# Kernel optimization log

Measured on AMD Instinct MI355X. Metric: run time of the kernel, lower is better.

The kernel has to match this reference:

```python
import jax, jax.numpy as jnp
import numpy as np

FEATURE_DIM = 128

def setup_inputs() -> dict:
    key0 = jax.random.key(0)
    k1, k2, k3 = jax.random.split(key0, 3)
    B, NQ, NK, D = 4, 4096, 4096, FEATURE_DIM
    return {
        "target": jax.random.normal(k1, (B, NQ, D), dtype=jnp.float32),
        "key": jax.random.normal(k2, (B, NK, D), dtype=jnp.float32),
        "value": jax.random.normal(k3, (B, NK, D), dtype=jnp.float32),
    }

def reference(target, key, value):
    # Lan_K F: scores = target @ key^T / sqrt(d); weights = softmax(scores); out = weights @ value
    scale = 1.0 / np.sqrt(FEATURE_DIM).astype(np.float32)
    scores = jnp.einsum('bqd,bkd->bqk', target, key) * scale  # [B, NQ, NK]
    weights = jax.nn.softmax(scores, axis=-1)
    return jnp.einsum('bqk,bkd->bqd', weights, value)  # [B, NQ, D]
```

## Files before the change

kernel.cpp:

```cpp
#include <hip/hip_runtime.h>
#include <stdint.h>

#define B_ 4
#define NQ_ 4096
#define NK_ 4096
#define D_ 128
#define BM_ 64
#define BN_ 128
#define NITER_ (NK_/BN_)
#define PS_ 136
#define OS_ 66

typedef __attribute__((ext_vector_type(8))) short short8;
typedef __attribute__((ext_vector_type(4))) float floatx4;
typedef unsigned int u32;

union frag_u { u32 u[4]; short8 s; };
union pair_u { u32 u[2]; uint2 v; };

__device__ __forceinline__ unsigned short f2bf_rne(float x){
  union { float f; u32 u; } c; c.f = x;
  u32 u = c.u;
  return (unsigned short)((u + 0x7fffu + ((u >> 16) & 1u)) >> 16);
}
__device__ __forceinline__ u32 pk2bf(float a, float b){
  union { float f; u32 u; } x, y; x.f = a; y.f = b;
  return ((x.u + 0x8000u) >> 16) | ((y.u + 0x8000u) & 0xffff0000u);
}

__global__ __launch_bounds__(256) void prep_kernel(
    const float* __restrict__ k, const float* __restrict__ v,
    unsigned short* __restrict__ kf, unsigned short* __restrict__ vf){
  __shared__ __align__(16) char smem[40960];
  const int t = threadIdx.x;
  const int blk = blockIdx.x;
  if (blk < 128){
    int b = blk >> 5, it = blk & 31;
    const float* src = k + ((size_t)b*NK_ + it*BN_)*D_;
    #pragma unroll
    for (int i = 0; i < 16; i++){
      int f = t + i*256;
      int row = f >> 5, c4 = f & 31;
      float4 a = *(const float4*)(src + (size_t)row*D_ + c4*4);
      ushort4 s;
      s.x = f2bf_rne(a.x); s.y = f2bf_rne(a.y);
      s.z = f2bf_rne(a.z); s.w = f2bf_rne(a.w);
      int kg = row >> 5, rem = row & 31;
      int dh = (rem >> 2) & 1;
      int l15 = ((rem >> 3) << 2) | (rem & 3);
      int wq = kg*2 + dh;
      int j = c4 >> 3, l4 = (c4 >> 1) & 3, half = c4 & 1;
      *(ushort4*)(smem + (wq*4 + j)*1088 + l4*272 + l15*16 + half*8) = s;
    }
    __syncthreads();
    unsigned short* dst = kf + (size_t)(b*32 + it)*2048*8;
    #pragma unroll
    for (int i = 0; i < 8; i++){
      int c = t + i*256;
      int lane = c & 63, j = (c >> 6) & 3, wq = c >> 8;
      int l15 = lane & 15, l4 = lane >> 4;
      short8 x = *(const short8*)(smem + (wq*4 + j)*1088 + l4*272 + l15*16);
      *(short8*)(dst + (size_t)c*8) = x;
    }
  } else {
    int blk2 = blk - 128;
    int b = blk2 >> 5, it = blk2 & 31;
    const float* src = v + ((size_t)b*NK_ + it*BN_)*D_;
    #pragma unroll
    for (int i = 0; i < 8; i++){
      int u2 = t + i*256;
      int rp = u2 >> 5, c4 = u2 & 31;
      int r0 = rp*2;
      const float* p0r = src + (size_t)r0*D_ + c4*4;
      float4 a0 = *(const float4*)p0r;
      float4 a1 = *(const float4*)(p0r + D_);
      int kk0 = r0 & 7;
      int l4a = (r0 >> 3) & 3, kga = r0 >> 5;
      float v0[4] = {a0.x, a0.y, a0.z, a0.w};
      float v1[4] = {a1.x, a1.y, a1.z, a1.w};
      #pragma unroll
      for (int jj = 0; jj < 4; jj++){
        int d = c4*4 + jj;
        int dh = d >> 6, dt = (d >> 4) & 3, l15 = d & 15;
        int c = ((kga*2 + dh)*4 + dt)*64 + l4a*16 + l15;
        ushort2 s2; s2.x = f2bf_rne(v0[jj]); s2.y = f2bf_rne(v1[jj]);
        *(ushort2*)(smem + c*16 + (c>>2)*16 + kk0*2) = s2;
      }
    }
    __syncthreads();
    unsigned short* dst = vf + (size_t)(b*32 + it)*2048*8;
    #pragma unroll
    for (int i = 0; i < 8; i++){
      int c = t + i*256;
      short8 x = *(const short8*)(smem + c*16 + (c>>2)*16);
      *(short8*)(dst + (size_t)c*8) = x;
    }
  }
}

__global__ __launch_bounds__(512, 2) void attn_kernel(
    const float* __restrict__ Qf, const unsigned short* __restrict__ Kb,
    const unsigned short* __restrict__ Vt, float* __restrict__ Out){
  __shared__ __align__(16) char sm[71680];
  unsigned short* smP = (unsigned short*)sm;
  float* smO = (float*)sm;
  float* smL = (float*)(sm + 69632);

  const int bi = blockIdx.x;
  const int b  = (bi >> 1) & 3;
  const int qt = ((bi >> 3) << 1) | (bi & 1);
  const int q0 = qt * BM_;
  const int tid = threadIdx.x;
  const int w = tid >> 6, lane = tid & 63;
  const int kg = w >> 1, dh = w & 1;
  const int l15 = lane & 15, l4 = lane >> 4;

  const short8* Kfrag = (const short8*)Kb;
  const short8* Vfrag = (const short8*)Vt;
  const size_t FSTRIDE = 8*4*64;
  const size_t fbase = (((size_t)b*32)*8 + w)*4*64 + lane;

  short8 qf[4][4];
  {
    const float* qp = Qf + ((size_t)b*NQ_ + q0)*D_;
    #pragma unroll
    for (int nb = 0; nb < 4; nb++)
      #pragma unroll
      for (int kbq = 0; kbq < 4; kbq++){
        const float* p = qp + (size_t)(nb*16 + l15)*D_ + kbq*32 + l4*8;
        float4 a = *(const float4*)p;
        float4 c4 = *(const float4*)(p + 4);
        frag_u f;
        f.u[0] = pk2bf(a.x, a.y);  f.u[1] = pk2bf(a.z, a.w);
        f.u[2] = pk2bf(c4.x, c4.y); f.u[3] = pk2bf(c4.z, c4.w);
        qf[nb][kbq] = f.s;
      }
  }

  short8 kfA[4], kfB[4], vfA[4], vfB[4];
  #pragma unroll
  for (int j = 0; j < 4; j++) kfA[j] = Kfrag[fbase + j*64];
  #pragma unroll
  for (int dt = 0; dt < 4; dt++) vfA[dt] = Vfrag[fbase + dt*64];
  #pragma unroll
  for (int j = 0; j < 4; j++) kfB[j] = Kfrag[fbase + FSTRIDE + j*64];
  #pragma unroll
  for (int dt = 0; dt < 4; dt++) vfB[dt] = Vfrag[fbase + FSTRIDE + dt*64];

  floatx4 o[4][4];
  #pragma unroll
  for (int nb = 0; nb < 4; nb++)
    #pragma unroll
    for (int dt = 0; dt < 4; dt++) o[nb][dt] = (floatx4)0.0f;
  float lsum[4] = {0.f, 0.f, 0.f, 0.f};

  const float SL = 0.08838834764831845f * 1.4426950408889634f;
  const size_t prow = (size_t)kg*32 + l4*8;

  for (int r = 0; r < NITER_/2; ++r){
    const int it = 2*r;
    unsigned short* bufA = smP + (size_t)(r & 1) * (2*64*PS_);
    unsigned short* bufB = bufA + 64*PS_;

    {
      floatx4 s[4];
      #pragma unroll
      for (int nb = 0; nb < 4; nb++){
        s[nb] = (floatx4)0.0f;
        s[nb] = __builtin_amdgcn_mfma_f32_16x16x32_bf16(kfA[0], qf[nb][0], s[nb], 0,0,0);
        s[nb] = __builtin_amdgcn_mfma_f32_16x16x32_bf16(kfA[1], qf[nb][1], s[nb], 0,0,0);
        s[nb] = __builtin_amdgcn_mfma_f32_16x16x32_bf16(kfA[2], qf[nb][2], s[nb], 0,0,0);
        s[nb] = __builtin_amdgcn_mfma_f32_16x16x32_bf16(kfA[3], qf[nb][3], s[nb], 0,0,0);
      }
      if (it + 2 < NITER_){
        #pragma unroll
        for (int j = 0; j < 4; j++)
          kfA[j] = Kfrag[fbase + (size_t)(it+2)*FSTRIDE + j*64];
      }
      #pragma unroll
      for (int nb = 0; nb < 4; nb++){
        float p0 = __builtin_amdgcn_exp2f(s[nb][0] * SL);
        float p1 = __builtin_amdgcn_exp2f(s[nb][1] * SL);
        float p2 = __builtin_amdgcn_exp2f(s[nb][2] * SL);
        float p3 = __builtin_amdgcn_exp2f(s[nb][3] * SL);
        lsum[nb] += (p0 + p1) + (p2 + p3);
        pair_u pp; pp.u[0] = pk2bf(p0, p1); pp.u[1] = pk2bf(p2, p3);
        *(uint2*)(bufA + (size_t)(nb*16 + l15)*PS_ + prow + dh*4) = pp.v;
      }
    }
    {
      floatx4 s[4];
      #pragma unroll
      for (int nb = 0; nb < 4; nb++){
        s[nb] = (floatx4)0.0f;
        s[nb] = __builtin_amdgcn_mfma_f32_16x16x32_bf16(kfB[0], qf[nb][0], s[nb], 0,0,0);
        s[nb] = __builtin_amdgcn_mfma_f32_16x16x32_bf16(kfB[1], qf[nb][1], s[nb], 0,0,0);
        s[nb] = __builtin_amdgcn_mfma_f32_16x16x32_bf16(kfB[2], qf[nb][2], s[nb], 0,0,0);
        s[nb] = __builtin_amdgcn_mfma_f32_16x16x32_bf16(kfB[3], qf[nb][3], s[nb], 0,0,0);
      }
      if (it + 3 < NITER_){
        #pragma unroll
        for (int j = 0; j < 4; j++)
          kfB[j] = Kfrag[fbase + (size_t)(it+3)*FSTRIDE + j*64];
      }
      #pragma unroll
      for (int nb = 0; nb < 4; nb++){
        float p0 = __builtin_amdgcn_exp2f(s[nb][0] * SL);
        float p1 = __builtin_amdgcn_exp2f(s[nb][1] * SL);
        float p2 = __builtin_amdgcn_exp2f(s[nb][2] * SL);
        float p3 = __builtin_amdgcn_exp2f(s[nb][3] * SL);
        lsum[nb] += (p0 + p1) + (p2 + p3);
        pair_u pp; pp.u[0] = pk2bf(p0, p1); pp.u[1] = pk2bf(p2, p3);
        *(uint2*)(bufB + (size_t)(nb*16 + l15)*PS_ + prow + dh*4) = pp.v;
      }
    }

    asm volatile("s_waitcnt lgkmcnt(0)" ::: "memory");
    __builtin_amdgcn_s_barrier();
    asm volatile("" ::: "memory");

    {
      short8 pf[4];
      #pragma unroll
      for (int nb = 0; nb < 4; nb++)
        pf[nb] = *(const short8*)(bufA + (size_t)(nb*16 + l15)*PS_ + prow);
      #pragma unroll
      for (int nb = 0; nb < 4; nb++)
        #pragma unroll
        for (int dt = 0; dt < 4; dt++)
          o[nb][dt] = __builtin_amdgcn_mfma_f32_16x16x32_bf16(pf[nb], vfA[dt], o[nb][dt], 0,0,0);
      if (it + 2 < NITER_){
        #pragma unroll
        for (int dt = 0; dt < 4; dt++)
          vfA[dt] = Vfrag[fbase + (size_t)(it+2)*FSTRIDE + dt*64];
      }
    }
    {
      short8 pf[4];
      #pragma unroll
      for (int nb = 0; nb < 4; nb++)
        pf[nb] = *(const short8*)(bufB + (size_t)(nb*16 + l15)*PS_ + prow);
      #pragma unroll
      for (int nb = 0; nb < 4; nb++)
        #pragma unroll
        for (int dt = 0; dt < 4; dt++)
          o[nb][dt] = __builtin_amdgcn_mfma_f32_16x16x32_bf16(pf[nb], vfB[dt], o[nb][dt], 0,0,0);
      if (it + 3 < NITER_){
        #pragma unroll
        for (int dt = 0; dt < 4; dt++)
          vfB[dt] = Vfrag[fbase + (size_t)(it+3)*FSTRIDE + dt*64];
      }
    }
  }

  #pragma unroll
  for (int nb = 0; nb < 4; nb++){
    float v = lsum[nb];
    v += __shfl_xor(v, 16);
    v += __shfl_xor(v, 32);
    lsum[nb] = v;
  }
  if (l4 == 0)
    #pragma unroll
    for (int nb = 0; nb < 4; nb++)
      smL[w*64 + nb*16 + l15] = lsum[nb];

  __syncthreads();

  if (w >= 4){
    float* r = smO + (size_t)(w - 4) * 4224;
    #pragma unroll
    for (int nb = 0; nb < 4; nb++)
      #pragma unroll
      for (int dt = 0; dt < 4; dt++)
        #pragma unroll
        for (int q = 0; q < 4; q++)
          r[(size_t)(nb*16 + l4*4 + q)*OS_ + dt*16 + l15] = o[nb][dt][q];
  }
  __syncthreads();
  if (w < 4){
    float* r = smO + (size_t)w * 4224;
    #pragma unroll
    for (int nb = 0; nb < 4; nb++)
      #pragma unroll
      for (int dt = 0; dt < 4; dt++)
        #pragma unroll
        for (int q = 0; q < 4; q++)
          o[nb][dt][q] += r[(size_t)(nb*16 + l4*4 + q)*OS_ + dt*16 + l15];
  }
  __syncthreads();
  if (w == 2 || w == 3){
    float* r = smO + (size_t)(w - 2) * 4224;
    #pragma unroll
    for (int nb = 0; nb < 4; nb++)
      #pragma unroll
      for (int dt = 0; dt < 4; dt++)
        #pragma unroll
        for (int q = 0; q < 4; q++)
          r[(size_t)(nb*16 + l4*4 + q)*OS_ + dt*16 + l15] = o[nb][dt][q];
  }
  __syncthreads();
  if (w < 2){
    float* r = smO + (size_t)w * 4224;
    float* og = Out + ((size_t)b*NQ_ + q0)*D_ + dh*64;
    #pragma unroll
    for (int nb = 0; nb < 4; nb++)
      #pragma unroll
      for (int q = 0; q < 4; q++){
        int row = nb*16 + l4*4 + q;
        float lt = 0.f;
        #pragma unroll
        for (int w2 = 0; w2 < 8; w2++) lt += smL[w2*64 + row];
        float inv = 1.0f / lt;
        #pragma unroll
        for (int dt = 0; dt < 4; dt++){
          float val = o[nb][dt][q] + r[(size_t)row*OS_ + dt*16 + l15];
          og[(size_t)row*D_ + dt*16 + l15] = val * inv;
        }
      }
  }
}

extern "C" void kernel_launch(void* const* d_in, const int* in_sizes, int n_in,
                              void* d_out, int out_size, void* d_ws, size_t ws_size,
                              hipStream_t stream){
  const float* q = (const float*)d_in[0];
  const float* k = (const float*)d_in[1];
  const float* v = (const float*)d_in[2];
  float* out = (float*)d_out;
  unsigned short* kb = (unsigned short*)d_ws;
  unsigned short* vt = kb + (size_t)B_*NK_*D_;
  prep_kernel<<<256, 256, 0, stream>>>(k, v, kb, vt);
  attn_kernel<<<256, 512, 0, stream>>>(q, kb, vt, out);
}
```

Measured before the change: 114.5 us.

## Split key dimension across two blocks with a combine kernel

Splits the key/value sequence into two halves handled by separate blocks, doubling the grid from 256 to 512 blocks. Each block writes unnormalized partial outputs and row sums to workspace, and a new combine kernel sums the two halves and normalizes. The softmax scale is also folded into Q before the bf16 conversion, which removes a multiply per score. The goal is better occupancy of the GPU's compute units. The cost is extra global traffic for the partials, one more kernel launch, and slightly different bf16 rounding of the scaled Q.

```diff
diff --git a/kernel.cpp b/kernel.cpp
--- a/kernel.cpp
+++ b/kernel.cpp
@@ -8,6 +8,8 @@
 #define BM_ 64
 #define BN_ 128
 #define NITER_ (NK_/BN_)
+#define NSPLIT_ 2
+#define NITH_ (NITER_/NSPLIT_)
 #define PS_ 136
 #define OS_ 66
 
@@ -100,15 +102,17 @@
 
 __global__ __launch_bounds__(512, 2) void attn_kernel(
     const float* __restrict__ Qf, const unsigned short* __restrict__ Kb,
-    const unsigned short* __restrict__ Vt, float* __restrict__ Out){
+    const unsigned short* __restrict__ Vt,
+    float* __restrict__ Op, float* __restrict__ Lp){
   __shared__ __align__(16) char sm[71680];
   unsigned short* smP = (unsigned short*)sm;
   float* smO = (float*)sm;
   float* smL = (float*)(sm + 69632);
 
   const int bi = blockIdx.x;
-  const int b  = (bi >> 1) & 3;
-  const int qt = ((bi >> 3) << 1) | (bi & 1);
+  const int b    = (bi >> 1) & 3;
+  const int half = (bi >> 3) & 1;
+  const int qt   = ((bi >> 4) << 1) | (bi & 1);
   const int q0 = qt * BM_;
   const int tid = threadIdx.x;
   const int w = tid >> 6, lane = tid & 63;
@@ -119,7 +123,9 @@
   const short8* Vfrag = (const short8*)Vt;
   const size_t FSTRIDE = 8*4*64;
   const size_t fbase = (((size_t)b*32)*8 + w)*4*64 + lane;
-
+  const int hbase = half * NITH_;
+
+  const float SL = 0.08838834764831845f * 1.4426950408889634f;
   short8 qf[4][4];
   {
     const float* qp = Qf + ((size_t)b*NQ_ + q0)*D_;
@@ -131,21 +137,21 @@
         float4 a = *(const float4*)p;
         float4 c4 = *(const float4*)(p + 4);
         frag_u f;
-        f.u[0] = pk2bf(a.x, a.y);  f.u[1] = pk2bf(a.z, a.w);
-        f.u[2] = pk2bf(c4.x, c4.y); f.u[3] = pk2bf(c4.z, c4.w);
+        f.u[0] = pk2bf(a.x*SL, a.y*SL);   f.u[1] = pk2bf(a.z*SL, a.w*SL);
+        f.u[2] = pk2bf(c4.x*SL, c4.y*SL); f.u[3] = pk2bf(c4.z*SL, c4.w*SL);
         qf[nb][kbq] = f.s;
       }
   }
 
   short8 kfA[4], kfB[4], vfA[4], vfB[4];
   #pragma unroll
-  for (int j = 0; j < 4; j++) kfA[j] = Kfrag[fbase + j*64];
-  #pragma unroll
-  for (int dt = 0; dt < 4; dt++) vfA[dt] = Vfrag[fbase + dt*64];
-  #pragma unroll
-  for (int j = 0; j < 4; j++) kfB[j] = Kfrag[fbase + FSTRIDE + j*64];
-  #pragma unroll
-  for (int dt = 0; dt < 4; dt++) vfB[dt] = Vfrag[fbase + FSTRIDE + dt*64];
+  for (int j = 0; j < 4; j++) kfA[j] = Kfrag[fbase + (size_t)hbase*FSTRIDE + j*64];
+  #pragma unroll
+  for (int dt = 0; dt < 4; dt++) vfA[dt] = Vfrag[fbase + (size_t)hbase*FSTRIDE + dt*64];
+  #pragma unroll
+  for (int j = 0; j < 4; j++) kfB[j] = Kfrag[fbase + (size_t)(hbase+1)*FSTRIDE + j*64];
+  #pragma unroll
+  for (int dt = 0; dt < 4; dt++) vfB[dt] = Vfrag[fbase + (size_t)(hbase+1)*FSTRIDE + dt*64];
 
   floatx4 o[4][4];
   #pragma unroll
@@ -154,11 +160,11 @@
     for (int dt = 0; dt < 4; dt++) o[nb][dt] = (floatx4)0.0f;
   float lsum[4] = {0.f, 0.f, 0.f, 0.f};
 
-  const float SL = 0.08838834764831845f * 1.4426950408889634f;
   const size_t prow = (size_t)kg*32 + l4*8;
 
-  for (int r = 0; r < NITER_/2; ++r){
-    const int it = 2*r;
+  for (int r = 0; r < NITH_/2; ++r){
+    const int lt = 2*r;
+    const int it = hbase + lt;
     unsigned short* bufA = smP + (size_t)(r & 1) * (2*64*PS_);
     unsigned short* bufB = bufA + 64*PS_;
 
@@ -172,17 +178,17 @@
         s[nb] = __builtin_amdgcn_mfma_f32_16x16x32_bf16(kfA[2], qf[nb][2], s[nb], 0,0,0);
         s[nb] = __builtin_amdgcn_mfma_f32_16x16x32_bf16(kfA[3], qf[nb][3], s[nb], 0,0,0);
       }
-      if (it + 2 < NITER_){
+      if (lt + 2 < NITH_){
         #pragma unroll
         for (int j = 0; j < 4; j++)
           kfA[j] = Kfrag[fbase + (size_t)(it+2)*FSTRIDE + j*64];
       }
       #pragma unroll
       for (int nb = 0; nb < 4; nb++){
-        float p0 = __builtin_amdgcn_exp2f(s[nb][0] * SL);
-        float p1 = __builtin_amdgcn_exp2f(s[nb][1] * SL);
-        float p2 = __builtin_amdgcn_exp2f(s[nb][2] * SL);
-        float p3 = __builtin_amdgcn_exp2f(s[nb][3] * SL);
+        float p0 = __builtin_amdgcn_exp2f(s[nb][0]);
+        float p1 = __builtin_amdgcn_exp2f(s[nb][1]);
+        float p2 = __builtin_amdgcn_exp2f(s[nb][2]);
+        float p3 = __builtin_amdgcn_exp2f(s[nb][3]);
         lsum[nb] += (p0 + p1) + (p2 + p3);
         pair_u pp; pp.u[0] = pk2bf(p0, p1); pp.u[1] = pk2bf(p2, p3);
         *(uint2*)(bufA + (size_t)(nb*16 + l15)*PS_ + prow + dh*4) = pp.v;
@@ -198,17 +204,17 @@
         s[nb] = __builtin_amdgcn_mfma_f32_16x16x32_bf16(kfB[2], qf[nb][2], s[nb], 0,0,0);
         s[nb] = __builtin_amdgcn_mfma_f32_16x16x32_bf16(kfB[3], qf[nb][3], s[nb], 0,0,0);
       }
-      if (it + 3 < NITER_){
+      if (lt + 3 < NITH_){
         #pragma unroll
         for (int j = 0; j < 4; j++)
           kfB[j] = Kfrag[fbase + (size_t)(it+3)*FSTRIDE + j*64];
       }
       #pragma unroll
       for (int nb = 0; nb < 4; nb++){
-        float p0 = __builtin_amdgcn_exp2f(s[nb][0] * SL);
-        float p1 = __builtin_amdgcn_exp2f(s[nb][1] * SL);
-        float p2 = __builtin_amdgcn_exp2f(s[nb][2] * SL);
-        float p3 = __builtin_amdgcn_exp2f(s[nb][3] * SL);
+        float p0 = __builtin_amdgcn_exp2f(s[nb][0]);
+        float p1 = __builtin_amdgcn_exp2f(s[nb][1]);
+        float p2 = __builtin_amdgcn_exp2f(s[nb][2]);
+        float p3 = __builtin_amdgcn_exp2f(s[nb][3]);
         lsum[nb] += (p0 + p1) + (p2 + p3);
         pair_u pp; pp.u[0] = pk2bf(p0, p1); pp.u[1] = pk2bf(p2, p3);
         *(uint2*)(bufB + (size_t)(nb*16 + l15)*PS_ + prow + dh*4) = pp.v;
@@ -229,7 +235,7 @@
         #pragma unroll
         for (int dt = 0; dt < 4; dt++)
           o[nb][dt] = __builtin_amdgcn_mfma_f32_16x16x32_bf16(pf[nb], vfA[dt], o[nb][dt], 0,0,0);
-      if (it + 2 < NITER_){
+      if (lt + 2 < NITH_){
         #pragma unroll
         for (int dt = 0; dt < 4; dt++)
           vfA[dt] = Vfrag[fbase + (size_t)(it+2)*FSTRIDE + dt*64];
@@ -245,7 +251,7 @@
         #pragma unroll
         for (int dt = 0; dt < 4; dt++)
           o[nb][dt] = __builtin_amdgcn_mfma_f32_16x16x32_bf16(pf[nb], vfB[dt], o[nb][dt], 0,0,0);
-      if (it + 3 < NITER_){
+      if (lt + 3 < NITH_){
         #pragma unroll
         for (int dt = 0; dt < 4; dt++)
           vfB[dt] = Vfrag[fbase + (size_t)(it+3)*FSTRIDE + dt*64];
@@ -302,7 +308,8 @@
   __syncthreads();
   if (w < 2){
     float* r = smO + (size_t)w * 4224;
-    float* og = Out + ((size_t)b*NQ_ + q0)*D_ + dh*64;
+    float* og = Op + (((size_t)half*B_ + b)*NQ_ + q0)*D_ + dh*64;
+    float* lg = Lp + ((size_t)half*B_ + b)*NQ_ + q0;
     #pragma unroll
     for (int nb = 0; nb < 4; nb++)
       #pragma unroll
@@ -311,14 +318,27 @@
         float lt = 0.f;
         #pragma unroll
         for (int w2 = 0; w2 < 8; w2++) lt += smL[w2*64 + row];
-        float inv = 1.0f / lt;
-        #pragma unroll
-        for (int dt = 0; dt < 4; dt++){
-          float val = o[nb][dt][q] + r[(size_t)row*OS_ + dt*16 + l15];
-          og[(size_t)row*D_ + dt*16 + l15] = val * inv;
-        }
-      }
-  }
+        if (dh == 0 && l15 == 0) lg[row] = lt;
+        #pragma unroll
+        for (int dt = 0; dt < 4; dt++)
+          og[(size_t)row*D_ + dt*16 + l15] = o[nb][dt][q] + r[(size_t)row*OS_ + dt*16 + l15];
+      }
+  }
+}
+
+__global__ __launch_bounds__(256) void combine_kernel(
+    const float* __restrict__ Op, const float* __restrict__ Lp,
+    float* __restrict__ Out){
+  int f = blockIdx.x * 256 + threadIdx.x;
+  size_t row = ((size_t)f * 4) / D_;
+  float4 a = ((const float4*)Op)[f];
+  float4 c = ((const float4*)(Op + (size_t)B_*NQ_*D_))[f];
+  float l = Lp[row] + Lp[(size_t)B_*NQ_ + row];
+  float inv = 1.0f / l;
+  float4 o;
+  o.x = (a.x + c.x) * inv; o.y = (a.y + c.y) * inv;
+  o.z = (a.z + c.z) * inv; o.w = (a.w + c.w) * inv;
+  ((float4*)Out)[f] = o;
 }
 
 extern "C" void kernel_launch(void* const* d_in, const int* in_sizes, int n_in,
@@ -330,6 +350,9 @@
   float* out = (float*)d_out;
   unsigned short* kb = (unsigned short*)d_ws;
   unsigned short* vt = kb + (size_t)B_*NK_*D_;
+  float* Op = (float*)((char*)d_ws + (size_t)8*1024*1024);
+  float* Lp = (float*)((char*)d_ws + (size_t)24*1024*1024);
   prep_kernel<<<256, 256, 0, stream>>>(k, v, kb, vt);
-  attn_kernel<<<256, 512, 0, stream>>>(q, kb, vt, out);
-}
+  attn_kernel<<<512, 512, 0, stream>>>(q, kb, vt, Op, Lp);
+  combine_kernel<<<2048, 256, 0, stream>>>(Op, Lp, out);
+}
```

New measurement: 130.9 us. 1.14x slower.
